# Kernel tuning notes

Measured on AMD Instinct MI355X. Metric: run time of the kernel, lower is better.

Reference implementation:

```python
import jax, jax.numpy as jnp
import numpy as np

B, S, D, H, DH = 4, 2048, 1024, 16, 64


def setup_inputs() -> dict:
    key = jax.random.key(0)
    ks = jax.random.split(key, 12)
    inp = {
        "query": jax.random.normal(ks[0], (B, S, D), jnp.float32),
        "key": jax.random.normal(ks[1], (B, S, D), jnp.float32),
        "value": jax.random.normal(ks[2], (B, S, D), jnp.float32),
        # causal mask, broadcast over batch and heads
        "mask": jnp.tril(jnp.ones((S, S), jnp.int32))[None, None, :, :],
        "Wq": jax.random.normal(ks[3], (D, D), jnp.float32) * 0.02,
        "bq": jnp.zeros((D,), jnp.float32),
        "Wk": jax.random.normal(ks[4], (D, D), jnp.float32) * 0.02,
        "bk": jnp.zeros((D,), jnp.float32),
        "Wv": jax.random.normal(ks[5], (D, D), jnp.float32) * 0.02,
        "bv": jnp.zeros((D,), jnp.float32),
        "Wo": jax.random.normal(ks[6], (D, D), jnp.float32) * 0.02,
        "bo": jnp.zeros((D,), jnp.float32),
    }
    return inp


def reference(query, key, value, mask, Wq, bq, Wk, bk, Wv, bv, Wo, bo):
    # linear projections (torch Linear: x @ W^T + b; here W stored as [in, out])
    q = query @ Wq + bq
    k = key @ Wk + bk
    v = value @ Wv + bv
    # [B, S, D] -> [B, H, S, DH]
    q = q.reshape(B, S, H, DH).transpose(0, 2, 1, 3)
    k = k.reshape(B, S, H, DH).transpose(0, 2, 1, 3)
    v = v.reshape(B, S, H, DH).transpose(0, 2, 1, 3)
    # materialized O(S^2) attention scores
    scores = jnp.einsum("bhqd,bhkd->bhqk", q, k) * (DH ** -0.5)
    scores = jnp.where(mask == 0, jnp.float32(-jnp.inf), scores)
    attn = jax.nn.softmax(scores, axis=-1)  # dropout is identity in eval
    x = jnp.einsum("bhqk,bhkd->bhqd", attn, v)
    # [B, H, S, DH] -> [B, S, D]
    x = x.transpose(0, 2, 1, 3).reshape(B, S, D)
    out = x @ Wo + bo
    return out
```

## Files before the change

kernel.cpp:

```cpp
#include <hip/hip_runtime.h>
#include <hip/hip_bf16.h>


typedef __bf16 bf16x8 __attribute__((ext_vector_type(8)));
typedef float f32x4 __attribute__((ext_vector_type(4)));

#define GLOBAL_AS __attribute__((address_space(1)))
#define LDS_AS __attribute__((address_space(3)))

#if __has_builtin(__builtin_amdgcn_exp2f)
#define EXP2(x) __builtin_amdgcn_exp2f(x)
#else
#define EXP2(x) __expf((x) * 0.6931471805599453f)
#endif
#define QSCALE 0.18033688f

static __device__ __forceinline__ unsigned short f2bf(float f) {
    __bf16 h = (__bf16)f;
    return __builtin_bit_cast(unsigned short, h);
}

static __device__ __forceinline__ void gload_lds16(const void* g, void* l) {
    __builtin_amdgcn_global_load_lds((const GLOBAL_AS void*)g, (LDS_AS void*)l, 16, 0, 0);
}

__global__ __launch_bounds__(256) void cvt3(const float* __restrict__ q,
                                            const float* __restrict__ k,
                                            const float* __restrict__ v,
                                            unsigned short* __restrict__ dq,
                                            unsigned short* __restrict__ dk,
                                            unsigned short* __restrict__ dv, int n8) {
    const int z = blockIdx.z;
    const float* src = (z == 0) ? q : (z == 1) ? k : v;
    unsigned short* dst = (z == 0) ? dq : (z == 1) ? dk : dv;
    int i = blockIdx.x * 256 + threadIdx.x;
    if (i >= n8) return;
    const float4* s = (const float4*)src + 2 * (size_t)i;
    float4 v0 = s[0], v1 = s[1];
    unsigned short h[8] = {f2bf(v0.x), f2bf(v0.y), f2bf(v0.z), f2bf(v0.w),
                           f2bf(v1.x), f2bf(v1.y), f2bf(v1.z), f2bf(v1.w)};
    *(uint4*)(dst + 8 * (size_t)i) = *(const uint4*)h;
}

__global__ void transpose_weights(const float* __restrict__ W0, const float* __restrict__ W1,
                                  const float* __restrict__ W2, const float* __restrict__ W3,
                                  unsigned short* __restrict__ T0, unsigned short* __restrict__ T1,
                                  unsigned short* __restrict__ T2, unsigned short* __restrict__ T3) {
    const float* W; unsigned short* T;
    switch (blockIdx.z) { case 0: W=W0; T=T0; break; case 1: W=W1; T=T1; break;
                          case 2: W=W2; T=T2; break; default: W=W3; T=T3; }
    __shared__ float tile[32][33];
    int tx = threadIdx.x, ty = threadIdx.y;
    int k0 = blockIdx.x * 32, n0 = blockIdx.y * 32;
#pragma unroll
    for (int j = 0; j < 4; j++) tile[ty + 8*j][tx] = W[(size_t)(k0 + ty + 8*j) * 1024 + n0 + tx];
    __syncthreads();
#pragma unroll
    for (int j = 0; j < 4; j++) T[(size_t)(n0 + ty + 8*j) * 1024 + k0 + tx] = f2bf(tile[tx][ty + 8*j]);
}

static __device__ __forceinline__ void gemm_core(const unsigned short* __restrict__ A,
                                                 const unsigned short* __restrict__ BT,
                                                 unsigned short* Asm, unsigned short* Bsm,
                                                 int rowBase, int colBase, int t,
                                                 f32x4 acc[4][4]) {
    const int lane = t & 63, w = t >> 6;
    const int g = lane >> 4, r16 = lane & 15;
    const int wr = w >> 1, wc = w & 1;
    const int K = 1024;
    const int srow = t >> 3;
    const int scol = (t & 7) * 8;

    const unsigned short* srcA[4];
    const unsigned short* srcB[4];
#pragma unroll
    for (int j = 0; j < 4; j++) {
        srcA[j] = A  + (size_t)(rowBase + srow + 32 * j) * K + scol;
        srcB[j] = BT + (size_t)(colBase + srow + 32 * j) * K + scol;
    }
    unsigned short* dstA = Asm + 512 * w;
    unsigned short* dstB = Bsm + 512 * w;

#pragma unroll
    for (int j = 0; j < 4; j++) {
        gload_lds16(srcA[j], dstA + 2048 * j);
        gload_lds16(srcB[j], dstB + 2048 * j);
    }
    __syncthreads();

    int cur = 0;
    for (int k0 = 0; k0 < K; k0 += 64) {
        if (k0 + 64 < K) {
            unsigned short* dA = dstA + (cur ^ 1) * 8192;
            unsigned short* dB = dstB + (cur ^ 1) * 8192;
#pragma unroll
            for (int j = 0; j < 4; j++) {
                gload_lds16(srcA[j] + k0 + 64, dA + 2048 * j);
                gload_lds16(srcB[j] + k0 + 64, dB + 2048 * j);
            }
        }
        const unsigned short* As = Asm + cur * 8192;
        const unsigned short* Bs = Bsm + cur * 8192;
#pragma unroll
        for (int ks = 0; ks < 2; ks++) {
            bf16x8 a[4], b[4];
#pragma unroll
            for (int m = 0; m < 4; m++) {
                int row = 64 * wr + 16 * m + r16;
                a[m] = *(const bf16x8*)(As + row * 64 + 32 * ks + 8 * g);
            }
#pragma unroll
            for (int n = 0; n < 4; n++) {
                int row = 64 * wc + 16 * n + r16;
                b[n] = *(const bf16x8*)(Bs + row * 64 + 32 * ks + 8 * g);
            }
#pragma unroll
            for (int m = 0; m < 4; m++)
#pragma unroll
                for (int n = 0; n < 4; n++)
                    acc[m][n] = __builtin_amdgcn_mfma_f32_16x16x32_bf16(a[m], b[n], acc[m][n], 0, 0, 0);
        }
        __syncthreads();
        cur ^= 1;
    }
}

__global__ __launch_bounds__(256) void gemm_qkv(
        const unsigned short* __restrict__ Xq, const unsigned short* __restrict__ Xk,
        const unsigned short* __restrict__ Xv,
        const unsigned short* __restrict__ WTq, const unsigned short* __restrict__ WTk,
        const unsigned short* __restrict__ WTv,
        const float* __restrict__ bq, const float* __restrict__ bk, const float* __restrict__ bv,
        unsigned short* __restrict__ Qb, unsigned short* __restrict__ Kb,
        unsigned short* __restrict__ VT) {
    __shared__ alignas(16) unsigned short Asm[2 * 8192];
    __shared__ alignas(16) unsigned short Bsm[2 * 8192];
    const int z = blockIdx.z;
    const unsigned short* A  = (z == 0) ? Xq : (z == 1) ? Xk : Xv;
    const unsigned short* BT = (z == 0) ? WTq : (z == 1) ? WTk : WTv;
    const float* bias        = (z == 0) ? bq : (z == 1) ? bk : bv;
    const int rowBase = blockIdx.y * 128, colBase = blockIdx.x * 128;
    const int t = threadIdx.x;
    const int lane = t & 63, w = t >> 6;
    const int g = lane >> 4, r16 = lane & 15;
    const int wr = w >> 1, wc = w & 1;

    f32x4 acc[4][4] = {};
    gemm_core(A, BT, Asm, Bsm, rowBase, colBase, t, acc);

    float bv4[4];
#pragma unroll
    for (int n = 0; n < 4; n++) bv4[n] = bias[colBase + 64 * wc + 16 * n + r16];

#pragma unroll
    for (int m = 0; m < 4; m++) {
#pragma unroll
        for (int n = 0; n < 4; n++) {
#pragma unroll
            for (int i = 0; i < 4; i++) {
                int row = rowBase + 64 * wr + 16 * m + 4 * g + i;
                int col = colBase + 64 * wc + 16 * n + r16;
                float v = acc[m][n][i] + bv4[n];
                int bidx = row >> 11, s = row & 2047;
                int hidx = col >> 6, dh = col & 63;
                size_t bh = (size_t)(bidx * 16 + hidx);
                if (z == 0)      Qb[(bh * 2048 + s) * 64 + dh] = f2bf(v * QSCALE);
                else if (z == 1) Kb[(bh * 2048 + s) * 64 + dh] = f2bf(v);
                else             VT[(bh * 64 + dh) * 2048 + s] = f2bf(v);
            }
        }
    }
}

__global__ __launch_bounds__(256) void gemm_out(const unsigned short* __restrict__ A,
                                                const unsigned short* __restrict__ BT,
                                                const float* __restrict__ bias,
                                                float* __restrict__ Out) {
    __shared__ alignas(16) unsigned short Asm[2 * 8192];
    __shared__ alignas(16) unsigned short Bsm[2 * 8192];
    const int rowBase = blockIdx.y * 128, colBase = blockIdx.x * 128;
    const int t = threadIdx.x;
    const int lane = t & 63, w = t >> 6;
    const int g = lane >> 4, r16 = lane & 15;
    const int wr = w >> 1, wc = w & 1;

    f32x4 acc[4][4] = {};
    gemm_core(A, BT, Asm, Bsm, rowBase, colBase, t, acc);

    float bv4[4];
#pragma unroll
    for (int n = 0; n < 4; n++) bv4[n] = bias[colBase + 64 * wc + 16 * n + r16];

#pragma unroll
    for (int m = 0; m < 4; m++)
#pragma unroll
        for (int n = 0; n < 4; n++)
#pragma unroll
            for (int i = 0; i < 4; i++) {
                int row = rowBase + 64 * wr + 16 * m + 4 * g + i;
                int col = colBase + 64 * wc + 16 * n + r16;
                Out[(size_t)row * 1024 + col] = acc[m][n][i] + bv4[n];
            }
}

static __device__ __forceinline__ void attn_step(
        const unsigned short* __restrict__ Ks, const unsigned short* __restrict__ Vs,
        const bf16x8 qfrag[2], f32x4 acco[4], float& m, float& lsum,
        int myq, int k0, bool diag,
        int g, int q16, int gh, int srcA, int srcB) {
    f32x4 accS[4] = {};
    __builtin_amdgcn_s_setprio(1);
#pragma unroll
    for (int ks = 0; ks < 2; ks++) {
#pragma unroll
        for (int tt = 0; tt < 4; tt++) {
            int row = 16 * tt + q16;
            bf16x8 ak = *(const bf16x8*)(Ks + row * 64 + ((4 * ks + g) ^ (row & 7)) * 8);
            accS[tt] = __builtin_amdgcn_mfma_f32_16x16x32_bf16(ak, qfrag[ks], accS[tt], 0, 0, 0);
        }
    }
    __builtin_amdgcn_s_setprio(0);

    float s[4][4];
#pragma unroll
    for (int tt = 0; tt < 4; tt++)
#pragma unroll
        for (int i = 0; i < 4; i++) {
            float v = accS[tt][i];
            if (diag) {
                int kg = k0 + 16 * tt + 4 * g + i;
                if (kg > myq) v = -1e30f;
            }
            s[tt][i] = v;
        }

    float pmax = s[0][0];
#pragma unroll
    for (int tt = 0; tt < 4; tt++)
#pragma unroll
        for (int i = 0; i < 4; i++) pmax = fmaxf(pmax, s[tt][i]);
    pmax = fmaxf(pmax, __shfl_xor(pmax, 16));
    pmax = fmaxf(pmax, __shfl_xor(pmax, 32));

    if (!__all(pmax <= m + 8.0f)) {
        float mnew = fmaxf(m, pmax);
        float sc = EXP2(m - mnew);
        lsum *= sc;
#pragma unroll
        for (int i = 0; i < 4; i++) {
            float sci = __shfl(sc, 4 * g + i);
#pragma unroll
            for (int d = 0; d < 4; d++) acco[d][i] *= sci;
        }
        m = mnew;
    }

    float tsum = 0.f;
    float p[4][4];
#pragma unroll
    for (int tt = 0; tt < 4; tt++)
#pragma unroll
        for (int i = 0; i < 4; i++) { p[tt][i] = EXP2(s[tt][i] - m); tsum += p[tt][i]; }
    tsum += __shfl_xor(tsum, 16);
    tsum += __shfl_xor(tsum, 32);
    lsum += tsum;

    unsigned lo[4], hi[4];
#pragma unroll
    for (int tt = 0; tt < 4; tt++) {
        lo[tt] = (unsigned)f2bf(p[tt][0]) | ((unsigned)f2bf(p[tt][1]) << 16);
        hi[tt] = (unsigned)f2bf(p[tt][2]) | ((unsigned)f2bf(p[tt][3]) << 16);
    }

#pragma unroll
    for (int ks = 0; ks < 2; ks++) {
        unsigned xa0 = __shfl(lo[2 * ks], srcA);
        unsigned xa1 = __shfl(hi[2 * ks], srcA);
        unsigned xa2 = __shfl(lo[2 * ks], srcB);
        unsigned xa3 = __shfl(hi[2 * ks], srcB);
        unsigned ya0 = __shfl(lo[2 * ks + 1], srcA);
        unsigned ya1 = __shfl(hi[2 * ks + 1], srcA);
        unsigned ya2 = __shfl(lo[2 * ks + 1], srcB);
        unsigned ya3 = __shfl(hi[2 * ks + 1], srcB);
        uint4 pw;
        pw.x = gh ? ya0 : xa0;
        pw.y = gh ? ya1 : xa1;
        pw.z = gh ? ya2 : xa2;
        pw.w = gh ? ya3 : xa3;
        bf16x8 pfrag = __builtin_bit_cast(bf16x8, pw);
        __builtin_amdgcn_s_setprio(1);
#pragma unroll
        for (int d = 0; d < 4; d++) {
            int row = 16 * d + q16;
            bf16x8 vv = *(const bf16x8*)(Vs + row * 64 + ((4 * ks + g) ^ (row & 7)) * 8);
            acco[d] = __builtin_amdgcn_mfma_f32_16x16x32_bf16(pfrag, vv, acco[d], 0, 0, 0);
        }
        __builtin_amdgcn_s_setprio(0);
    }
}

__global__ __launch_bounds__(256) void attn_kernel(const unsigned short* __restrict__ Q,
                                                   const unsigned short* __restrict__ Kb,
                                                   const unsigned short* __restrict__ VT,
                                                   unsigned short* __restrict__ Xout) {
    __shared__ alignas(16) unsigned short Ksm[2][4096];
    __shared__ alignas(16) unsigned short Vsm[2][4096];
    const int t = threadIdx.x;
    const int lane = t & 63, w = t >> 6;
    const int g = lane >> 4, q16 = lane & 15;
    const int bh = blockIdx.y;
    const int b = bh >> 4, h = bh & 15;

    const int srow0 = t >> 3;
    const int ssrc = ((t & 7) ^ (srow0 & 7)) * 8;
    const unsigned short* srcK[2];
    const unsigned short* srcV[2];
#pragma unroll
    for (int j = 0; j < 2; j++) {
        int row = srow0 + 32 * j;
        srcK[j] = Kb + ((size_t)bh * 2048 + row) * 64 + ssrc;
        srcV[j] = VT + ((size_t)bh * 64 + row) * 2048 + ssrc;
    }

    const int gh = g >> 1;
    const int g0 = 2 * (g & 1);
    const int srcA = 16 * g0 + q16, srcB = srcA + 16;

#pragma unroll 1
    for (int ph = 0; ph < 2; ph++) {
        const int qt = ph ? (31 - (int)blockIdx.x) : (int)blockIdx.x;
        const int q0 = qt * 64;
        const int myq = q0 + 16 * w + q16;
        const int nkt = qt + 1;

        bf16x8 qfrag[2];
        {
            const uint4* qp = (const uint4*)(Q + ((size_t)bh * 2048 + myq) * 64);
            qfrag[0] = __builtin_bit_cast(bf16x8, qp[g]);
            qfrag[1] = __builtin_bit_cast(bf16x8, qp[4 + g]);
        }

        f32x4 acco[4] = {};
        float m = -1e30f, lsum = 0.f;
        int cur = 0;

#pragma unroll
        for (int j = 0; j < 2; j++) {
            gload_lds16(srcK[j], &Ksm[0][512 * w + 2048 * j]);
            gload_lds16(srcV[j], &Vsm[0][512 * w + 2048 * j]);
        }
        __syncthreads();

        for (int kt = 0; kt < nkt; kt++) {
            if (kt + 1 < nkt) {
                int nxt = cur ^ 1;
#pragma unroll
                for (int j = 0; j < 2; j++) {
                    gload_lds16(srcK[j] + (size_t)(kt + 1) * 4096, &Ksm[nxt][512 * w + 2048 * j]);
                    gload_lds16(srcV[j] + (size_t)(kt + 1) * 64,   &Vsm[nxt][512 * w + 2048 * j]);
                }
            }
            attn_step(Ksm[cur], Vsm[cur], qfrag, acco, m, lsum,
                      myq, kt * 64, kt == nkt - 1, g, q16, gh, srcA, srcB);
            __syncthreads();
            cur ^= 1;
        }

#pragma unroll
        for (int i = 0; i < 4; i++) {
            float li = __shfl(lsum, 4 * g + i);
            float inv = 1.f / li;
            int row = q0 + 16 * w + 4 * g + i;
#pragma unroll
            for (int d = 0; d < 4; d++) {
                int col = h * 64 + 16 * d + q16;
                Xout[((size_t)b * 2048 + row) * 1024 + col] = f2bf(acco[d][i] * inv);
            }
        }
        __syncthreads();
    }
}

extern "C" void kernel_launch(void* const* d_in, const int* in_sizes, int n_in,
                              void* d_out, int out_size, void* d_ws, size_t ws_size,
                              hipStream_t stream) {
    (void)in_sizes; (void)n_in; (void)out_size; (void)ws_size;
    const float* query = (const float*)d_in[0];
    const float* key   = (const float*)d_in[1];
    const float* value = (const float*)d_in[2];
    const float* Wq = (const float*)d_in[4];
    const float* bq = (const float*)d_in[5];
    const float* Wk = (const float*)d_in[6];
    const float* bk = (const float*)d_in[7];
    const float* Wv = (const float*)d_in[8];
    const float* bv = (const float*)d_in[9];
    const float* Wo = (const float*)d_in[10];
    const float* bo = (const float*)d_in[11];

    char* base = (char*)d_ws;
    const size_t MB = 1u << 20;
    unsigned short* WTq = (unsigned short*)(base + 0 * MB);
    unsigned short* WTk = (unsigned short*)(base + 2 * MB);
    unsigned short* WTv = (unsigned short*)(base + 4 * MB);
    unsigned short* WTo = (unsigned short*)(base + 6 * MB);
    unsigned short* Qb  = (unsigned short*)(base + 8 * MB);
    unsigned short* Kbf = (unsigned short*)(base + 24 * MB);
    unsigned short* VTb = (unsigned short*)(base + 40 * MB);
    unsigned short* X   = (unsigned short*)(base + 56 * MB);

    unsigned short* Xk = (unsigned short*)d_out;
    unsigned short* Xv = Xk + (size_t)8192 * 1024;

    const int n8 = (8192 * 1024) / 8;

    transpose_weights<<<dim3(32, 32, 4), dim3(32, 8), 0, stream>>>(Wq, Wk, Wv, Wo, WTq, WTk, WTv, WTo);
    cvt3<<<dim3(4096, 1, 3), 256, 0, stream>>>(query, key, value, X, Xk, Xv, n8);
    gemm_qkv<<<dim3(8, 64, 3), 256, 0, stream>>>(X, Xk, Xv, WTq, WTk, WTv, bq, bk, bv, Qb, Kbf, VTb);
    attn_kernel<<<dim3(16, 64), 256, 0, stream>>>(Qb, Kbf, VTb, X);
    gemm_out<<<dim3(8, 64), 256, 0, stream>>>(X, WTo, bo, (float*)d_out);
}
```

Measured before the change: 373.7 us.

## Swizzle GEMM LDS tiles and stage V transpose through shared memory

Applies an XOR swizzle to the column chunk index of the A/B tiles in LDS, both on async global-to-LDS loads and on MFMA fragment reads, to reduce bank conflicts. For the V projection, the epilogue writes the tile transposed into LDS and then emits coalesced 16-byte stores to VT, replacing strided 2-byte scattered stores. This adds an extra barrier and LDS traffic in the V epilogue.

New measurement: 344.2 us. 1.09x faster.

```diff
diff --git a/kernel.cpp b/kernel.cpp
--- a/kernel.cpp
+++ b/kernel.cpp
@@ -69,7 +69,7 @@
     const int wr = w >> 1, wc = w & 1;
     const int K = 1024;
     const int srow = t >> 3;
-    const int scol = (t & 7) * 8;
+    const int scol = ((t & 7) ^ ((t >> 3) & 7)) * 8;
 
     const unsigned short* srcA[4];
     const unsigned short* srcB[4];
@@ -107,12 +107,12 @@
 #pragma unroll
             for (int m = 0; m < 4; m++) {
                 int row = 64 * wr + 16 * m + r16;
-                a[m] = *(const bf16x8*)(As + row * 64 + 32 * ks + 8 * g);
+                a[m] = *(const bf16x8*)(As + row * 64 + ((4 * ks + g) ^ (row & 7)) * 8);
             }
 #pragma unroll
             for (int n = 0; n < 4; n++) {
                 int row = 64 * wc + 16 * n + r16;
-                b[n] = *(const bf16x8*)(Bs + row * 64 + 32 * ks + 8 * g);
+                b[n] = *(const bf16x8*)(Bs + row * 64 + ((4 * ks + g) ^ (row & 7)) * 8);
             }
 #pragma unroll
             for (int m = 0; m < 4; m++)
@@ -133,8 +133,9 @@
         const float* __restrict__ bq, const float* __restrict__ bk, const float* __restrict__ bv,
         unsigned short* __restrict__ Qb, unsigned short* __restrict__ Kb,
         unsigned short* __restrict__ VT) {
-    __shared__ alignas(16) unsigned short Asm[2 * 8192];
-    __shared__ alignas(16) unsigned short Bsm[2 * 8192];
+    __shared__ alignas(16) unsigned short smem[32768];
+    unsigned short* Asm = smem;
+    unsigned short* Bsm = smem + 16384;
     const int z = blockIdx.z;
     const unsigned short* A  = (z == 0) ? Xq : (z == 1) ? Xk : Xv;
     const unsigned short* BT = (z == 0) ? WTq : (z == 1) ? WTk : WTv;
@@ -152,21 +153,49 @@
 #pragma unroll
     for (int n = 0; n < 4; n++) bv4[n] = bias[colBase + 64 * wc + 16 * n + r16];
 
-#pragma unroll
-    for (int m = 0; m < 4; m++) {
-#pragma unroll
-        for (int n = 0; n < 4; n++) {
-#pragma unroll
-            for (int i = 0; i < 4; i++) {
-                int row = rowBase + 64 * wr + 16 * m + 4 * g + i;
-                int col = colBase + 64 * wc + 16 * n + r16;
-                float v = acc[m][n][i] + bv4[n];
-                int bidx = row >> 11, s = row & 2047;
-                int hidx = col >> 6, dh = col & 63;
-                size_t bh = (size_t)(bidx * 16 + hidx);
-                if (z == 0)      Qb[(bh * 2048 + s) * 64 + dh] = f2bf(v * QSCALE);
-                else if (z == 1) Kb[(bh * 2048 + s) * 64 + dh] = f2bf(v);
-                else             VT[(bh * 64 + dh) * 2048 + s] = f2bf(v);
+    if (z == 2) {
+        const int TS = 136;
+        unsigned short* Tsm = smem;
+#pragma unroll
+        for (int m = 0; m < 4; m++) {
+#pragma unroll
+            for (int n = 0; n < 4; n++) {
+                int c = 64 * wc + 16 * n + r16;
+                int r = 64 * wr + 16 * m + 4 * g;
+                unsigned short pk[4];
+#pragma unroll
+                for (int i = 0; i < 4; i++) pk[i] = f2bf(acc[m][n][i] + bv4[n]);
+                *(uint2*)(Tsm + c * TS + r) = *(const uint2*)pk;
+            }
+        }
+        __syncthreads();
+        const int bidx = rowBase >> 11;
+        const int sBase = rowBase & 2047;
+        const int sloc = (t & 15) * 8;
+#pragma unroll
+        for (int jj = 0; jj < 8; jj++) {
+            int dloc = (t >> 4) + 16 * jj;
+            uint4 v = *(const uint4*)(Tsm + dloc * TS + sloc);
+            int col = colBase + dloc;
+            int hidx = col >> 6, dh = col & 63;
+            *(uint4*)&VT[(((size_t)(bidx * 16 + hidx)) * 64 + dh) * 2048 + sBase + sloc] = v;
+        }
+    } else {
+#pragma unroll
+        for (int m = 0; m < 4; m++) {
+#pragma unroll
+            for (int n = 0; n < 4; n++) {
+#pragma unroll
+                for (int i = 0; i < 4; i++) {
+                    int row = rowBase + 64 * wr + 16 * m + 4 * g + i;
+                    int col = colBase + 64 * wc + 16 * n + r16;
+                    float v = acc[m][n][i] + bv4[n];
+                    int bidx = row >> 11, s = row & 2047;
+                    int hidx = col >> 6, dh = col & 63;
+                    size_t bh = (size_t)(bidx * 16 + hidx);
+                    if (z == 0) Qb[(bh * 2048 + s) * 64 + dh] = f2bf(v * QSCALE);
+                    else        Kb[(bh * 2048 + s) * 64 + dh] = f2bf(v);
+                }
             }
         }
     }
@@ -176,8 +205,9 @@
                                                 const unsigned short* __restrict__ BT,
                                                 const float* __restrict__ bias,
                                                 float* __restrict__ Out) {
-    __shared__ alignas(16) unsigned short Asm[2 * 8192];
-    __shared__ alignas(16) unsigned short Bsm[2 * 8192];
+    __shared__ alignas(16) unsigned short smem[32768];
+    unsigned short* Asm = smem;
+    unsigned short* Bsm = smem + 16384;
     const int rowBase = blockIdx.y * 128, colBase = blockIdx.x * 128;
     const int t = threadIdx.x;
     const int lane = t & 63, w = t >> 6;
```
